# Performance work log

Measured on AMD Instinct MI355X. Metric: run time of the kernel, lower is better.

The kernel has to match this reference:

```python
import jax, jax.numpy as jnp
import numpy as np

EPS = 1e-5  # torch InstanceNorm2d default eps


def conv1x1(x, w, b):
    # x: [B,C,H,W], w: [O,C], b: [O]
    return jnp.einsum('bchw,oc->bohw', x, w) + b[None, :, None, None]


def conv3x3(x, w, b):
    y = jax.lax.conv_general_dilated(x, w, (1, 1), 'SAME',
                                     dimension_numbers=('NCHW', 'OIHW', 'NCHW'))
    return y + b[None, :, None, None]


def inorm(x):
    # InstanceNorm2d, affine=False, biased variance
    m = jnp.mean(x, axis=(2, 3), keepdims=True)
    v = jnp.var(x, axis=(2, 3), keepdims=True)
    return (x - m) * jax.lax.rsqrt(v + EPS)


def self_attn(x, wq, bq, wk, bk, wv, bv, gamma):
    B, C, H, W = x.shape
    N = H * W
    q = conv1x1(x, wq, bq).reshape(B, -1, N)   # [B,C/8,N]
    k = conv1x1(x, wk, bk).reshape(B, -1, N)   # [B,C/8,N]
    A = jax.nn.softmax(jnp.einsum('bdn,bdm->bnm', q, k), axis=-1)  # [B,N,N]
    v = conv1x1(x, wv, bv).reshape(B, C, N)    # [B,C,N]
    out = jnp.einsum('bcm,bnm->bcn', v, A).reshape(B, C, H, W)
    return gamma * out + x


def setup_inputs() -> dict:
    key = jax.random.key(0)
    B, C, H, W = 2, 256, 64, 64
    C8 = C // 8
    ks = iter(jax.random.split(key, 40))

    def n(shape, scale=0.05):
        return jax.random.normal(next(ks), shape, dtype=jnp.float32) * scale

    inp = {
        'x': jax.random.normal(next(ks), (B, C, H, W), dtype=jnp.float32),
        'y': jax.random.normal(next(ks), (B, C, H, W), dtype=jnp.float32),
    }
    for p in ('sa1', 'sa2', 'top'):
        inp[p + '_wq'] = n((C8, C)); inp[p + '_bq'] = n((C8,))
        inp[p + '_wk'] = n((C8, C)); inp[p + '_bk'] = n((C8,))
        inp[p + '_wv'] = n((C, C));  inp[p + '_bv'] = n((C,))
        inp[p + '_gamma'] = n((1,), 0.1)
    inp['conv1_w'] = n((C, C, 3, 3)); inp['conv1_b'] = n((C,))
    inp['conv2_w'] = n((C, C, 3, 3)); inp['conv2_b'] = n((C,))
    return inp


def reference(x, y,
              sa1_wq, sa1_bq, sa1_wk, sa1_bk, sa1_wv, sa1_bv, sa1_gamma,
              sa2_wq, sa2_bq, sa2_wk, sa2_bk, sa2_wv, sa2_bv, sa2_gamma,
              top_wq, top_bq, top_wk, top_bk, top_wv, top_bv, top_gamma,
              conv1_w, conv1_b, conv2_w, conv2_b):
    out_1 = inorm(self_attn(x, sa1_wq, sa1_bq, sa1_wk, sa1_bk, sa1_wv, sa1_bv, sa1_gamma))
    out_2 = inorm(out_1 + conv3x3(out_1, conv1_w, conv1_b))
    out_3 = inorm(self_attn(y, sa2_wq, sa2_bq, sa2_wk, sa2_bk, sa2_wv, sa2_bv, sa2_gamma))

    B, C, H, W = out_2.shape
    N = H * W
    q = conv1x1(out_2, top_wq, top_bq).reshape(B, -1, N)
    k = conv1x1(out_2, top_wk, top_bk).reshape(B, -1, N)
    A = jax.nn.softmax(jnp.einsum('bdn,bdm->bnm', q, k), axis=-1)
    v = conv1x1(out_3, top_wv, top_bv).reshape(B, C, N)
    out = jnp.einsum('bcm,bnm->bcn', v, A).reshape(B, C, H, W)
    out = top_gamma * out + y
    out = inorm(out)
    out = inorm(out + out_3)
    out_4 = conv3x3(out, conv2_w, conv2_b)
    out = inorm(out + out_4)
    return out
```

## Files before the change

kernel.cpp:

```cpp
#include <hip/hip_runtime.h>
#include <hip/hip_bf16.h>

typedef __hip_bfloat16 bf16;
typedef __attribute__((ext_vector_type(8))) short s8v;
typedef __attribute__((ext_vector_type(4))) float f4v;

#define NPIX 4096
#define CDIM 256
#define MN_ELEMS (1 << 20)
#define QKVSTR (320L * NPIX)
#define QKTSTR (64L * NPIX)

typedef __attribute__((address_space(1))) const unsigned int g_u32;
typedef __attribute__((address_space(3))) unsigned int l_u32;
__device__ __forceinline__ void glds16(const void* g, void* l) {
  __builtin_amdgcn_global_load_lds((g_u32*)g, (l_u32*)l, 16, 0, 0);
}

__device__ inline s8v ld8(const bf16* p) { return *(const s8v*)p; }
__device__ inline s8v ld8(const float* p) {
  float4 f0 = *(const float4*)p;
  float4 f1 = *(const float4*)(p + 4);
  s8v r; bf16* e = (bf16*)&r;
  e[0] = __float2bfloat16(f0.x); e[1] = __float2bfloat16(f0.y);
  e[2] = __float2bfloat16(f0.z); e[3] = __float2bfloat16(f0.w);
  e[4] = __float2bfloat16(f1.x); e[5] = __float2bfloat16(f1.y);
  e[6] = __float2bfloat16(f1.z); e[7] = __float2bfloat16(f1.w);
  return r;
}

template<int NT>
__global__ __launch_bounds__(256) void fattn_k(
    const bf16* __restrict__ qkt, const bf16* __restrict__ Vg,
    bf16* __restrict__ out)
{
  constexpr int SN = NT / 32;
  __shared__ bf16 k_s[128 * 32];
  __shared__ bf16 v_s[4 * 128 * 32];
  __shared__ bf16 p_s[4 * NT * 32];
  float* sums = (float*)k_s;

  const int tid = threadIdx.x;
  const int z = blockIdx.z;
  const int w = tid >> 6, lane = tid & 63;
  const int l15 = lane & 15, oct = lane >> 4;
  const int wr = w >> 1, wc = w & 1;
  const int n0 = blockIdx.x * NT, c0 = blockIdx.y * 128;
  const bf16* qk = qkt + (long)z * QKTSTR;
  const bf16* Vz = Vg + (long)z * QKVSTR;
  const int srow = lane >> 2, scol = (lane & 3) * 8;

  #pragma unroll
  for (int g = 0; g < NT / 64; ++g)
    glds16(qk + (long)(n0 + g * 64 + (w << 4) + srow) * 64 + scol,
           p_s + g * 2048 + w * 512);
  glds16(qk + (long)((w << 4) + srow) * 64 + 32 + scol, k_s + w * 512);
  glds16(qk + (long)(64 + (w << 4) + srow) * 64 + 32 + scol, k_s + 2048 + w * 512);
  #pragma unroll
  for (int g = 0; g < 8; ++g) {
    const int kk = g & 3, rg = g >> 2;
    glds16(Vz + (long)(c0 + rg * 64 + (w << 4) + srow) * 4096 + kk * 32 + scol,
           v_s + kk * 4096 + rg * 2048 + w * 512);
  }
  __syncthreads();

  s8v qf[SN];
  #pragma unroll
  for (int st = 0; st < SN; ++st)
    qf[st] = *(const s8v*)(p_s + (wr * (NT / 2) + st * 16 + l15) * 32 + oct * 8);
  __syncthreads();

  f4v acc[4][SN];
  #pragma unroll
  for (int i = 0; i < 4; ++i)
    #pragma unroll
    for (int j = 0; j < SN; ++j) acc[i][j] = (f4v){0.f, 0.f, 0.f, 0.f};
  float rs[SN][4];
  #pragma unroll
  for (int st = 0; st < SN; ++st)
    #pragma unroll
    for (int r = 0; r < 4; ++r) rs[st][r] = 0.f;

  for (int i = 0; i < 32; ++i) {
    s8v kf[4];
    #pragma unroll
    for (int nt = 0; nt < 4; ++nt)
      kf[nt] = *(const s8v*)(k_s + (wc * 64 + nt * 16 + l15) * 32 + oct * 8);
    #pragma unroll
    for (int st = 0; st < SN; ++st) {
      f4v sa[4];
      #pragma unroll
      for (int nt = 0; nt < 4; ++nt) {
        f4v zz = (f4v){0.f, 0.f, 0.f, 0.f};
        sa[nt] = __builtin_amdgcn_mfma_f32_16x16x32_bf16(qf[st], kf[nt], zz, 0, 0, 0);
      }
      const int nrow = wr * (NT / 2) + st * 16 + oct * 4;
      #pragma unroll
      for (int nt = 0; nt < 4; ++nt) {
        const int kk = wc * 2 + (nt >> 1);
        const int mc = ((nt & 1) << 4) + l15;
        bf16* pw = p_s + kk * (NT * 32) + nrow * 32 + mc;
        #pragma unroll
        for (int r = 0; r < 4; ++r) {
          float e = __expf(sa[nt][r]);
          rs[st][r] += e;
          pw[r * 32] = __float2bfloat16(e);
        }
      }
    }
    __syncthreads();
    #pragma unroll
    for (int kk = 0; kk < 4; ++kk) {
      s8v vf[4], pf[SN];
      #pragma unroll
      for (int st = 0; st < 4; ++st)
        vf[st] = *(const s8v*)(v_s + kk * 4096 + (wr * 64 + st * 16 + l15) * 32 + oct * 8);
      #pragma unroll
      for (int nt = 0; nt < SN; ++nt)
        pf[nt] = *(const s8v*)(p_s + kk * (NT * 32) + (wc * (NT / 2) + nt * 16 + l15) * 32 + oct * 8);
      #pragma unroll
      for (int st = 0; st < 4; ++st)
        #pragma unroll
        for (int nt = 0; nt < SN; ++nt)
          acc[st][nt] = __builtin_amdgcn_mfma_f32_16x16x32_bf16(vf[st], pf[nt], acc[st][nt], 0, 0, 0);
    }
    __syncthreads();
    if (i < 31) {
      const int m1 = (i + 1) * 128;
      glds16(qk + (long)(m1 + (w << 4) + srow) * 64 + 32 + scol, k_s + w * 512);
      glds16(qk + (long)(m1 + 64 + (w << 4) + srow) * 64 + 32 + scol, k_s + 2048 + w * 512);
      #pragma unroll
      for (int g = 0; g < 8; ++g) {
        const int kk = g & 3, rg = g >> 2;
        glds16(Vz + (long)(c0 + rg * 64 + (w << 4) + srow) * 4096 + m1 + kk * 32 + scol,
               v_s + kk * 4096 + rg * 2048 + w * 512);
      }
      __syncthreads();
    }
  }

  #pragma unroll
  for (int st = 0; st < SN; ++st)
    #pragma unroll
    for (int r = 0; r < 4; ++r) {
      #pragma unroll
      for (int s = 1; s < 16; s <<= 1) rs[st][r] += __shfl_xor(rs[st][r], s);
    }
  if (l15 == 0) {
    #pragma unroll
    for (int st = 0; st < SN; ++st)
      #pragma unroll
      for (int r = 0; r < 4; ++r)
        sums[wc * NT + wr * (NT / 2) + st * 16 + oct * 4 + r] = rs[st][r];
  }
  __syncthreads();

  float rinv[SN];
  #pragma unroll
  for (int nt = 0; nt < SN; ++nt) {
    const int n = wc * (NT / 2) + nt * 16 + l15;
    rinv[nt] = 1.f / (sums[n] + sums[NT + n]);
  }
  bf16* op = out + (long)z * ((long)CDIM * NPIX);
  #pragma unroll
  for (int st = 0; st < 4; ++st) {
    const int gc = c0 + wr * 64 + st * 16 + oct * 4;
    #pragma unroll
    for (int nt = 0; nt < SN; ++nt) {
      const int gn = n0 + wc * (NT / 2) + nt * 16 + l15;
      #pragma unroll
      for (int r = 0; r < 4; ++r)
        op[(long)(gc + r) * NPIX + gn] = __float2bfloat16(acc[st][nt][r] * rinv[nt]);
    }
  }
}

__global__ __launch_bounds__(256) void gemm128(
    const bf16* __restrict__ A, const bf16* __restrict__ Bm,
    bf16* __restrict__ Cp, int N, int K, int nchunk, int nsplit,
    long abat, long bbat)
{
  __shared__ bf16 a_s0[128 * 32], a_s1[128 * 32];
  __shared__ bf16 b_s0[128 * 32], b_s1[128 * 32];
  const int tid = threadIdx.x;
  const int z = blockIdx.z;
  const int bb = z / nsplit, ks = z - bb * nsplit;
  A  += bb * abat;
  Bm += bb * bbat;
  const int w = tid >> 6, lane = tid & 63;
  const int l15 = lane & 15, oct = lane >> 4;
  const int wr = w >> 1, wc = w & 1;
  const int m0 = blockIdx.y * 128, n0 = blockIdx.x * 128;
  const int kc0 = ks * nchunk, kc1 = kc0 + nchunk;

  const int srow = lane >> 2, skoff = (lane & 3) * 8;
  const long aRow0 = (long)(m0 + (w << 4) + srow) * K;
  const long aRow1 = (long)(m0 + ((w + 4) << 4) + srow) * K;
  const long bRow0 = (long)(n0 + (w << 4) + srow) * K;
  const long bRow1 = (long)(n0 + ((w + 4) << 4) + srow) * K;
  const int ldsOff0 = (w) * 512, ldsOff1 = (w + 4) * 512;

  f4v acc[4][4];
  #pragma unroll
  for (int i = 0; i < 4; ++i)
    #pragma unroll
    for (int j = 0; j < 4; ++j) acc[i][j] = (f4v){0.f, 0.f, 0.f, 0.f};

  for (int kc = kc0; kc < kc1; ++kc) {
    const int kb0 = kc * 64 + skoff;
    const int kb1 = kb0 + 32;
    glds16(A + aRow0 + kb0, a_s0 + ldsOff0);
    glds16(A + aRow1 + kb0, a_s0 + ldsOff1);
    glds16(A + aRow0 + kb1, a_s1 + ldsOff0);
    glds16(A + aRow1 + kb1, a_s1 + ldsOff1);
    glds16(Bm + bRow0 + kb0, b_s0 + ldsOff0);
    glds16(Bm + bRow1 + kb0, b_s0 + ldsOff1);
    glds16(Bm + bRow0 + kb1, b_s1 + ldsOff0);
    glds16(Bm + bRow1 + kb1, b_s1 + ldsOff1);
    __syncthreads();
    #pragma unroll
    for (int h = 0; h < 2; ++h) {
      const bf16* as = h ? a_s1 : a_s0;
      const bf16* bs = h ? b_s1 : b_s0;
      s8v af[4], bfv[4];
      #pragma unroll
      for (int st = 0; st < 4; ++st)
        af[st] = *(const s8v*)(as + (wr * 64 + st * 16 + l15) * 32 + oct * 8);
      #pragma unroll
      for (int nt = 0; nt < 4; ++nt)
        bfv[nt] = *(const s8v*)(bs + (wc * 64 + nt * 16 + l15) * 32 + oct * 8);
      #pragma unroll
      for (int st = 0; st < 4; ++st)
        #pragma unroll
        for (int nt = 0; nt < 4; ++nt)
          acc[st][nt] = __builtin_amdgcn_mfma_f32_16x16x32_bf16(af[st], bfv[nt], acc[st][nt], 0, 0, 0);
    }
    __syncthreads();
  }

  bf16* Cz = Cp + (long)z * ((long)gridDim.y * 128) * N;
  #pragma unroll
  for (int st = 0; st < 4; ++st) {
    const int gm = m0 + wr * 64 + st * 16 + oct * 4;
    #pragma unroll
    for (int nt = 0; nt < 4; ++nt) {
      const int gn = n0 + wc * 64 + nt * 16 + l15;
      #pragma unroll
      for (int r = 0; r < 4; ++r)
        Cz[(long)(gm + r) * N + gn] = __float2bfloat16(acc[st][nt][r]);
    }
  }
}

template<int QKT, typename TBe>
__global__ __launch_bounds__(256) void proj_k(
    const float* __restrict__ A, const float* __restrict__ A2,
    const TBe* __restrict__ B1, const TBe* __restrict__ B2,
    const float* __restrict__ bias, const float* __restrict__ bias2,
    bf16* __restrict__ Cm, bf16* __restrict__ qkt,
    int M, int N, int K, long bbat, long cbat, int nchunk)
{
  __shared__ bf16 a_s[64][40];
  __shared__ bf16 b_s[64][40];
  const int tid = threadIdx.x;
  const int z = blockIdx.z, stage = z >> 1, bat = z & 1;
  const float* Au = stage ? A2 : A;
  const float* biasu = stage ? bias2 : bias;
  const TBe* Bm = (stage ? B2 : B1) + bat * bbat;
  Cm += z * cbat;
  if (QKT) qkt += z * QKTSTR;
  const int m0 = blockIdx.y * 64, n0 = blockIdx.x * 64;
  const int w = tid >> 6, lane = tid & 63;
  const int l15 = lane & 15, oct = lane >> 4;

  f4v acc[4];
  #pragma unroll
  for (int i = 0; i < 4; ++i) acc[i] = (f4v){0.f, 0.f, 0.f, 0.f};

  const int a_i0 = tid >> 2, a_i1 = (tid & 3) * 8;
  const int b_i0 = tid >> 3, b_i1 = (tid & 7) * 8;

  s8v pa, pb;
  auto ldA = [&](int kc, s8v& d) {
    if (m0 + a_i0 < M) d = ld8(Au + (long)(m0 + a_i0) * K + kc * 32 + a_i1);
    else d = (s8v){0,0,0,0,0,0,0,0};
  };
  auto ldB = [&](int kc, s8v& d) {
    d = ld8(Bm + (long)(kc * 32 + b_i0) * N + n0 + b_i1);
  };

  ldA(0, pa); ldB(0, pb);
  for (int kc = 0; kc < nchunk; ++kc) {
    *(s8v*)&a_s[a_i0][a_i1] = pa;
    {
      const bf16* e = (const bf16*)&pb;
      #pragma unroll
      for (int j = 0; j < 8; ++j) b_s[b_i1 + j][b_i0] = e[j];
    }
    __syncthreads();
    if (kc + 1 < nchunk) { ldA(kc + 1, pa); ldB(kc + 1, pb); }
    s8v af = *(const s8v*)&a_s[w * 16 + l15][oct * 8];
    #pragma unroll
    for (int nt = 0; nt < 4; ++nt) {
      s8v bfr = *(const s8v*)&b_s[nt * 16 + l15][oct * 8];
      acc[nt] = __builtin_amdgcn_mfma_f32_16x16x32_bf16(af, bfr, acc[nt], 0, 0, 0);
    }
    __syncthreads();
  }
  const int gm_base = m0 + w * 16 + oct * 4;
  #pragma unroll
  for (int nt = 0; nt < 4; ++nt) {
    const int gn = n0 + nt * 16 + l15;
    #pragma unroll
    for (int r = 0; r < 4; ++r) {
      int gm = gm_base + r;
      if (gm < M) {
        float vv = acc[nt][r] + biasu[gm];
        if (QKT && gm < 64) qkt[(long)gn * 64 + gm] = __float2bfloat16(vv);
        else Cm[(long)gm * N + gn] = __float2bfloat16(vv);
      }
    }
  }
}

__global__ __launch_bounds__(256) void reduce_bias_k(
    const bf16* __restrict__ part, const float* __restrict__ bias,
    bf16* __restrict__ out, int nsplit)
{
  const int g8 = (blockIdx.x * 256 + threadIdx.x) * 8;
  const int b = g8 >> 20, i = g8 & (MN_ELEMS - 1);
  const bf16* p0 = part + (long)b * nsplit * MN_ELEMS + i;
  float s[8];
  { s8v v = *(const s8v*)p0; const bf16* e = (const bf16*)&v;
    #pragma unroll
    for (int j = 0; j < 8; ++j) s[j] = __bfloat162float(e[j]); }
  for (int p = 1; p < nsplit; ++p) {
    s8v v = *(const s8v*)(p0 + (long)p * MN_ELEMS); const bf16* e = (const bf16*)&v;
    #pragma unroll
    for (int j = 0; j < 8; ++j) s[j] += __bfloat162float(e[j]);
  }
  float bv = bias[i >> 12];
  s8v o; bf16* eo = (bf16*)&o;
  #pragma unroll
  for (int j = 0; j < 8; ++j) eo[j] = __float2bfloat16(s[j] + bv);
  *(s8v*)(out + g8) = o;
}

__global__ __launch_bounds__(256) void cat_k(
    const float* __restrict__ wq, const float* __restrict__ bq,
    const float* __restrict__ wk, const float* __restrict__ bk,
    const float* __restrict__ wv, const float* __restrict__ bv,
    float* __restrict__ wcat, float* __restrict__ bcat, int M)
{
  int idx = blockIdx.x * 256 + threadIdx.x;
  int total = M << 8;
  if (idx < total) {
    int r = idx >> 8, c = idx & 255;
    float v;
    if (r < 32) v = wq[r * 256 + c];
    else if (r < 64) v = wk[(r - 32) * 256 + c];
    else v = wv[(r - 64) * 256 + c];
    wcat[idx] = v;
  } else if (idx < total + M) {
    int r = idx - total;
    bcat[r] = (r < 32) ? bq[r] : (r < 64) ? bk[r - 32] : bv[r - 64];
  }
}

__global__ __launch_bounds__(256) void cvtw2_k(
    const float* __restrict__ w1, const float* __restrict__ w2,
    bf16* __restrict__ o1, bf16* __restrict__ o2)
{
  const float* in = blockIdx.y ? w2 : w1;
  bf16* out = blockIdx.y ? o2 : o1;
  int idx = blockIdx.x * 256 + threadIdx.x;
  int o = idx / 2304, r = idx % 2304;
  int j = r >> 8, c = r & 255;
  out[idx] = __float2bfloat16(in[(o * 256 + c) * 9 + j]);
}

__global__ __launch_bounds__(256) void im2colT2_k(const bf16* __restrict__ x,
                                                  bf16* __restrict__ colT)
{
  __shared__ bf16 lds[3 * 66 * 66];
  const int tid = threadIdx.x;
  const int h = blockIdx.x, c0 = blockIdx.y * 64;
  x    += (long)blockIdx.z * CDIM * NPIX;
  colT += (long)blockIdx.z * 2304L * NPIX;

  if (tid < 192) {
    int row = tid >> 6, c = tid & 63;
    lds[(row * 66 + 0) * 66 + c] = __float2bfloat16(0.f);
    lds[(row * 66 + 65) * 66 + c] = __float2bfloat16(0.f);
  }
  const int w2 = tid & 31, chi = tid >> 5;
  #pragma unroll
  for (int it = 0; it < 24; ++it) {
    int row = it >> 3, cg = it & 7;
    int c = cg * 8 + chi;
    int hh = h + row - 1;
    unsigned int pix = 0;
    if ((unsigned)hh < 64u)
      pix = *(const unsigned int*)(x + (long)(c0 + c) * 4096 + hh * 64 + w2 * 2);
    const bf16* pp = (const bf16*)&pix;
    lds[(row * 66 + (w2 * 2 + 1)) * 66 + c] = pp[0];
    lds[(row * 66 + (w2 * 2 + 2)) * 66 + c] = pp[1];
  }
  __syncthreads();
  const int cg8 = tid & 7, wq = tid >> 3;
  #pragma unroll
  for (int j = 0; j < 9; ++j) {
    const int dy = j / 3, dx = j % 3;
    #pragma unroll
    for (int half = 0; half < 2; ++half) {
      int w = wq + half * 32;
      s8v v = *(const s8v*)&lds[(dy * 66 + (w + dx)) * 66 + cg8 * 8];
      *(s8v*)(colT + (long)(h * 64 + w) * 2304 + j * 256 + c0 + cg8 * 8) = v;
    }
  }
}

__device__ inline void ld16(const bf16* p, float* v) {
  s8v r0 = *(const s8v*)p, r1 = *(const s8v*)(p + 8);
  const bf16* e0 = (const bf16*)&r0; const bf16* e1 = (const bf16*)&r1;
  #pragma unroll
  for (int j = 0; j < 8; ++j) { v[j] = __bfloat162float(e0[j]); v[8 + j] = __bfloat162float(e1[j]); }
}
__device__ inline void ld16(const float* p, float* v) {
  #pragma unroll
  for (int q = 0; q < 4; ++q) {
    float4 f = *(const float4*)(p + q * 4);
    v[q * 4 + 0] = f.x; v[q * 4 + 1] = f.y; v[q * 4 + 2] = f.z; v[q * 4 + 3] = f.w;
  }
}
__device__ inline void st16(bf16* p, const float* v) {
  s8v o0, o1v; bf16* f0 = (bf16*)&o0; bf16* f1 = (bf16*)&o1v;
  #pragma unroll
  for (int j = 0; j < 8; ++j) { f0[j] = __float2bfloat16(v[j]); f1[j] = __float2bfloat16(v[8 + j]); }
  *(s8v*)p = o0; *(s8v*)(p + 8) = o1v;
}
__device__ inline void st16(float* p, const float* v) {
  #pragma unroll
  for (int q = 0; q < 4; ++q) {
    float4 f; f.x = v[q * 4 + 0]; f.y = v[q * 4 + 1]; f.z = v[q * 4 + 2]; f.w = v[q * 4 + 3];
    *(float4*)(p + q * 4) = f;
  }
}

template<typename TAe, typename TBe, typename TOe, int G>
__global__ __launch_bounds__(256) void inorm_k(
    const TAe* __restrict__ a, const TBe* __restrict__ b,
    const float* __restrict__ g, TOe* __restrict__ out)
{
  __shared__ float red[8];
  const int tid = threadIdx.x;
  const long base = (long)blockIdx.x * NPIX + tid * 16;
  float gv = G ? *g : 1.f;
  float va[16], vbv[16], v[16];
  ld16(a + base, va);
  ld16(b + base, vbv);
  #pragma unroll
  for (int j = 0; j < 16; ++j) v[j] = gv * va[j] + vbv[j];
  float sum = 0.f, sq = 0.f;
  #pragma unroll
  for (int j = 0; j < 16; ++j) { sum += v[j]; sq += v[j] * v[j]; }
  #pragma unroll
  for (int s = 32; s; s >>= 1) { sum += __shfl_xor(sum, s); sq += __shfl_xor(sq, s); }
  if ((tid & 63) == 0) { red[tid >> 6] = sum; red[4 + (tid >> 6)] = sq; }
  __syncthreads();
  sum = red[0] + red[1] + red[2] + red[3];
  sq  = red[4] + red[5] + red[6] + red[7];
  float mean = sum * (1.f / NPIX);
  float var  = fmaxf(sq * (1.f / NPIX) - mean * mean, 0.f);
  float rstd = rsqrtf(var + 1e-5f);
  float o[16];
  #pragma unroll
  for (int j = 0; j < 16; ++j) o[j] = (v[j] - mean) * rstd;
  st16(out + base, o);
}

static const long CN = (long)CDIM * NPIX;

static void attn_core(int nb, bf16* qkv, bf16* qkt, bf16* t0, hipStream_t stream)
{
  fattn_k<64><<<dim3(64, 2, nb), dim3(256), 0, stream>>>(qkt, qkv + 64 * NPIX, t0);
}

static void run_conv(const bf16* src, const bf16* wcvt, const float* cb,
                     bf16* colT, bf16* part, bf16* dst, hipStream_t stream)
{
  dim3 TB(256);
  im2colT2_k<<<dim3(64, 4, 2), TB, 0, stream>>>(src, colT);
  gemm128<<<dim3(32, 2, 8), TB, 0, stream>>>(wcvt, colT, part, NPIX, 2304, 9, 4,
                                             0L, 2304L * NPIX);
  reduce_bias_k<<<dim3(1024), TB, 0, stream>>>(part, cb, dst, 4);
}

extern "C" void kernel_launch(void* const* d_in, const int* in_sizes, int n_in,
                              void* d_out, int out_size, void* d_ws, size_t ws_size,
                              hipStream_t stream)
{
  (void)in_sizes; (void)n_in; (void)out_size; (void)ws_size;
  const float* x = (const float*)d_in[0];
  const float* y = (const float*)d_in[1];
  auto W = [&](int i) { return (const float*)d_in[i]; };

  char* wp = (char*)d_ws;
  auto take = [&](size_t nbytes) { char* p = wp; wp += (nbytes + 255) & ~(size_t)255; return p; };
  bf16*  qkv   = (bf16*)take((size_t)4 * QKVSTR * 2);
  bf16*  qkt   = (bf16*)take((size_t)4 * QKTSTR * 2);
  bf16*  t0    = (bf16*)take((size_t)4 * CN * 2);
  bf16*  u1    = (bf16*)take(2 * CN * 2);
  bf16*  u2    = (bf16*)take(2 * CN * 2);
  bf16*  u3    = (bf16*)take(2 * CN * 2);
  bf16*  u4    = (bf16*)take(2 * CN * 2);
  bf16*  colT  = (bf16*)take((size_t)2 * 2304L * NPIX * 2);
  bf16*  wcvt1 = (bf16*)take((size_t)589824 * 2);
  bf16*  wcvt2 = (bf16*)take((size_t)589824 * 2);
  float* wcat1 = (float*)take((size_t)81920 * 4);
  float* bcat1 = (float*)take(320 * 4);
  float* wcat2 = (float*)take((size_t)81920 * 4);
  float* bcat2 = (float*)take(320 * 4);
  float* wqk   = (float*)take((size_t)16384 * 4);
  float* bqk   = (float*)take(64 * 4);
  bf16*  part  = (bf16*)take((size_t)8 * MN_ELEMS * 2);
  bf16*  cvout = qkv;

  dim3 TB(256);

  cat_k<<<dim3(322), TB, 0, stream>>>(W(2), W(3), W(4), W(5), W(6), W(7), wcat1, bcat1, 320);
  cat_k<<<dim3(322), TB, 0, stream>>>(W(9), W(10), W(11), W(12), W(13), W(14), wcat2, bcat2, 320);
  cat_k<<<dim3(65),  TB, 0, stream>>>(W(16), W(17), W(18), W(19), nullptr, nullptr, wqk, bqk, 64);
  cvtw2_k<<<dim3(2304, 2), TB, 0, stream>>>(W(23), W(25), wcvt1, wcvt2);

  proj_k<1,float><<<dim3(64,5,4), TB, 0, stream>>>(
      wcat1, wcat2, x, y, bcat1, bcat2, qkv, qkt, 320, NPIX, 256, CN, QKVSTR, 8);
  attn_core(4, qkv, qkt, t0, stream);

  inorm_k<bf16,float,bf16,1><<<dim3(512), TB, 0, stream>>>(t0, x, W(8), u1);
  inorm_k<bf16,float,bf16,1><<<dim3(512), TB, 0, stream>>>(t0 + 2 * CN, y, W(15), u3);

  run_conv(u1, wcvt1, W(24), colT, part, cvout, stream);
  inorm_k<bf16,bf16,bf16,0><<<dim3(512), TB, 0, stream>>>(u1, cvout, nullptr, u2);

  proj_k<1,bf16><<<dim3(64,1,2), TB, 0, stream>>>(
      wqk, wqk, u2, u2, bqk, bqk, qkv, qkt, 64, NPIX, 256, CN, QKVSTR, 8);
  proj_k<0,bf16><<<dim3(64,4,2), TB, 0, stream>>>(
      W(20), W(20), u3, u3, W(21), W(21), qkv + 64 * NPIX, qkt, 256, NPIX, 256, CN, QKVSTR, 8);
  attn_core(2, qkv, qkt, t0, stream);
  inorm_k<bf16,float,bf16,1><<<dim3(512), TB, 0, stream>>>(t0, y, W(22), u1);
  inorm_k<bf16,bf16,bf16,0><<<dim3(512), TB, 0, stream>>>(u1, u3, nullptr, u4);
  run_conv(u4, wcvt2, W(26), colT, part, cvout, stream);
  inorm_k<bf16,bf16,float,0><<<dim3(512), TB, 0, stream>>>(u4, cvout, nullptr, (float*)d_out);
}
```

Baseline: 407.9 us.

## Transpose score MFMA, swizzle P tile in LDS, use exp2 with pre-scaled Q

The QK^T MFMA now takes its operands in swapped order, so each lane holds four consecutive key columns for one query row. The exp'd probabilities are packed into one 8-byte LDS store with an XOR swizzle, replacing four scalar bf16 stores, and the PV read is swizzled to match. Q is pre-multiplied by log2(e) in the projection epilogue so the softmax can use the native exp2. Row sums shrink to one per lane, reduced with two shuffles instead of four, and s_setprio is raised around the MFMA bursts. Together these aim to cut LDS store instructions, bank conflicts and exp/reduction ALU work in the attention inner loop, at the cost of more complex indexing.

```diff
diff --git a/kernel.cpp b/kernel.cpp
--- a/kernel.cpp
+++ b/kernel.cpp
@@ -3,6 +3,7 @@
 
 typedef __hip_bfloat16 bf16;
 typedef __attribute__((ext_vector_type(8))) short s8v;
+typedef __attribute__((ext_vector_type(4))) short s4v;
 typedef __attribute__((ext_vector_type(4))) float f4v;
 
 #define NPIX 4096
@@ -10,6 +11,12 @@
 #define MN_ELEMS (1 << 20)
 #define QKVSTR (320L * NPIX)
 #define QKTSTR (64L * NPIX)
+
+#if __has_builtin(__builtin_amdgcn_exp2f)
+#define EXP2F(x) __builtin_amdgcn_exp2f(x)
+#else
+#define EXP2F(x) exp2f(x)
+#endif
 
 typedef __attribute__((address_space(1))) const unsigned int g_u32;
 typedef __attribute__((address_space(3))) unsigned int l_u32;
@@ -75,11 +82,9 @@
   for (int i = 0; i < 4; ++i)
     #pragma unroll
     for (int j = 0; j < SN; ++j) acc[i][j] = (f4v){0.f, 0.f, 0.f, 0.f};
-  float rs[SN][4];
-  #pragma unroll
-  for (int st = 0; st < SN; ++st)
-    #pragma unroll
-    for (int r = 0; r < 4; ++r) rs[st][r] = 0.f;
+  float rs[SN];
+  #pragma unroll
+  for (int st = 0; st < SN; ++st) rs[st] = 0.f;
 
   for (int i = 0; i < 32; ++i) {
     s8v kf[4];
@@ -88,24 +93,31 @@
       kf[nt] = *(const s8v*)(k_s + (wc * 64 + nt * 16 + l15) * 32 + oct * 8);
     #pragma unroll
     for (int st = 0; st < SN; ++st) {
+      const int n = wr * (NT / 2) + st * 16 + l15;
+      const int sw = ((n >> 1) & 3) << 4;
       f4v sa[4];
+      __builtin_amdgcn_s_setprio(1);
       #pragma unroll
       for (int nt = 0; nt < 4; ++nt) {
         f4v zz = (f4v){0.f, 0.f, 0.f, 0.f};
-        sa[nt] = __builtin_amdgcn_mfma_f32_16x16x32_bf16(qf[st], kf[nt], zz, 0, 0, 0);
+        sa[nt] = __builtin_amdgcn_mfma_f32_16x16x32_bf16(kf[nt], qf[st], zz, 0, 0, 0);
       }
-      const int nrow = wr * (NT / 2) + st * 16 + oct * 4;
+      __builtin_amdgcn_s_setprio(0);
       #pragma unroll
       for (int nt = 0; nt < 4; ++nt) {
         const int kk = wc * 2 + (nt >> 1);
-        const int mc = ((nt & 1) << 4) + l15;
-        bf16* pw = p_s + kk * (NT * 32) + nrow * 32 + mc;
+        int byte = kk * (NT * 64) + n * 64 + (nt & 1) * 32 + oct * 8;
+        byte ^= sw;
+        s4v pk; bf16* pe = (bf16*)&pk;
+        float rsum = 0.f;
         #pragma unroll
         for (int r = 0; r < 4; ++r) {
-          float e = __expf(sa[nt][r]);
-          rs[st][r] += e;
-          pw[r * 32] = __float2bfloat16(e);
+          float e = EXP2F(sa[nt][r]);
+          rsum += e;
+          pe[r] = __float2bfloat16(e);
         }
+        rs[st] += rsum;
+        *(s4v*)((char*)p_s + byte) = pk;
       }
     }
     __syncthreads();
@@ -116,13 +128,19 @@
       for (int st = 0; st < 4; ++st)
         vf[st] = *(const s8v*)(v_s + kk * 4096 + (wr * 64 + st * 16 + l15) * 32 + oct * 8);
       #pragma unroll
-      for (int nt = 0; nt < SN; ++nt)
-        pf[nt] = *(const s8v*)(p_s + kk * (NT * 32) + (wc * (NT / 2) + nt * 16 + l15) * 32 + oct * 8);
+      for (int nt = 0; nt < SN; ++nt) {
+        const int n = wc * (NT / 2) + nt * 16 + l15;
+        int byte = kk * (NT * 64) + n * 64 + oct * 16;
+        byte ^= ((n >> 1) & 3) << 4;
+        pf[nt] = *(const s8v*)((const char*)p_s + byte);
+      }
+      __builtin_amdgcn_s_setprio(1);
       #pragma unroll
       for (int st = 0; st < 4; ++st)
         #pragma unroll
         for (int nt = 0; nt < SN; ++nt)
           acc[st][nt] = __builtin_amdgcn_mfma_f32_16x16x32_bf16(vf[st], pf[nt], acc[st][nt], 0, 0, 0);
+      __builtin_amdgcn_s_setprio(0);
     }
     __syncthreads();
     if (i < 31) {
@@ -140,18 +158,14 @@
   }
 
   #pragma unroll
-  for (int st = 0; st < SN; ++st)
-    #pragma unroll
-    for (int r = 0; r < 4; ++r) {
-      #pragma unroll
-      for (int s = 1; s < 16; s <<= 1) rs[st][r] += __shfl_xor(rs[st][r], s);
-    }
-  if (l15 == 0) {
+  for (int st = 0; st < SN; ++st) {
+    rs[st] += __shfl_xor(rs[st], 16);
+    rs[st] += __shfl_xor(rs[st], 32);
+  }
+  if (lane < 16) {
     #pragma unroll
     for (int st = 0; st < SN; ++st)
-      #pragma unroll
-      for (int r = 0; r < 4; ++r)
-        sums[wc * NT + wr * (NT / 2) + st * 16 + oct * 4 + r] = rs[st][r];
+      sums[wc * NT + wr * (NT / 2) + st * 16 + l15] = rs[st];
   }
   __syncthreads();
 
@@ -316,8 +330,12 @@
       int gm = gm_base + r;
       if (gm < M) {
         float vv = acc[nt][r] + biasu[gm];
-        if (QKT && gm < 64) qkt[(long)gn * 64 + gm] = __float2bfloat16(vv);
-        else Cm[(long)gm * N + gn] = __float2bfloat16(vv);
+        if (QKT && gm < 64) {
+          float vv2 = (gm < 32) ? vv * 1.44269504f : vv;
+          qkt[(long)gn * 64 + gm] = __float2bfloat16(vv2);
+        } else {
+          Cm[(long)gm * N + gn] = __float2bfloat16(vv);
+        }
       }
     }
   }
```

Measured after the change: 396.0 us. -2.9%, faster.
